# Kernel tuning notes

Measured on AMD Instinct MI355X. Metric: run time of the kernel, lower is better.

The kernel has to match this reference:

```python
import jax, jax.numpy as jnp
import numpy as np

NUM_BINS = 8
C_OUT = 64
CA_RED = 8  # channel-attention reduction (CBAM default-style)


def _bn(x, g, b):
    # BatchNorm1d in training mode: batch statistics, eps=1e-3
    mu = x.mean(0)
    var = x.var(0)
    return (x - mu) / jnp.sqrt(var + 1e-3) * g + b


def setup_inputs() -> dict:
    key = jax.random.key(0)
    ks = jax.random.split(key, 20)
    Nv, U = 400000, 200000
    s = 0.05
    inp = {
        'voxel_features': jax.random.normal(ks[0], (Nv, 5), jnp.float32),
        'voxel_features_coords': jax.random.randint(ks[1], (Nv, 4), 0, NUM_BINS),
        'v_feat_unq_coords': jax.random.randint(ks[2], (U,), 0, 1000000),
        'v_feat_unq_inv': jax.random.randint(ks[3], (Nv,), 0, U),
        'v_feat_unq_cnt': jax.random.randint(ks[4], (U,), 0, 5),
        # up_dimension: Linear(5,32)+ReLU, Linear(32,64)
        'up_w1': jax.random.normal(ks[5], (5, C_OUT // 2), jnp.float32) * s,
        'up_b1': jnp.zeros((C_OUT // 2,), jnp.float32),
        'up_w2': jax.random.normal(ks[6], (C_OUT // 2, C_OUT), jnp.float32) * s,
        'up_b2': jnp.zeros((C_OUT,), jnp.float32),
        # ZBAM (CBAM-1d): channel-attention shared MLP + spatial conv k=7
        'ca_w1': jax.random.normal(ks[7], (C_OUT, C_OUT // CA_RED), jnp.float32) * s,
        'ca_w2': jax.random.normal(ks[8], (C_OUT // CA_RED, C_OUT), jnp.float32) * s,
        'sa_conv': jax.random.normal(ks[9], (1, 2, 7), jnp.float32) * s,  # OIH
        # bin_shuffle: Linear(512,256,no bias)+BN+ReLU, Linear(256,64,no bias)+BN+ReLU
        'bs_w1': jax.random.normal(ks[10], (C_OUT * NUM_BINS, C_OUT * NUM_BINS // 2), jnp.float32) * s,
        'bn1_g': jnp.ones((C_OUT * NUM_BINS // 2,), jnp.float32),
        'bn1_b': jnp.zeros((C_OUT * NUM_BINS // 2,), jnp.float32),
        'bs_w2': jax.random.normal(ks[11], (C_OUT * NUM_BINS // 2, C_OUT), jnp.float32) * s,
        'bn2_g': jnp.ones((C_OUT,), jnp.float32),
        'bn2_b': jnp.zeros((C_OUT,), jnp.float32),
    }
    return inp


def reference(voxel_features, voxel_features_coords, v_feat_unq_coords,
              v_feat_unq_inv, v_feat_unq_cnt,
              up_w1, up_b1, up_w2, up_b2,
              ca_w1, ca_w2, sa_conv,
              bs_w1, bn1_g, bn1_b, bs_w2, bn2_g, bn2_b):
    coords = voxel_features_coords
    U = v_feat_unq_coords.shape[0]
    binz = coords[:, 1]
    # --- binning: scatter voxels into (pillar, z-bin) slots ---
    src = jnp.zeros((U, NUM_BINS, 6), jnp.float32)
    src = src.at[v_feat_unq_inv, binz, 1:].set(voxel_features)
    src = src.at[:, :, 0].set(-1.0)
    src = src.at[v_feat_unq_inv, binz, 0].set(coords[:, 0].astype(jnp.float32))
    # --- occupancy mask + compaction (eager nonzero) ---
    idx = jnp.nonzero(v_feat_unq_cnt >= 2)[0]
    src = src[idx]                      # (N, P=8, 6)
    feat = src[:, :, 1:]                # (N, 8, 5)
    # --- up_dimension MLP ---
    h = jnp.maximum(feat @ up_w1 + up_b1, 0.0) @ up_w2 + up_b2  # (N, 8, 64)
    x = jnp.swapaxes(h, 1, 2)           # (N, C=64, P=8)
    # --- ZBAM: CBAM-style channel + spatial attention over z-bins ---
    def ca_mlp(v):
        return jnp.maximum(v @ ca_w1, 0.0) @ ca_w2
    ca = jax.nn.sigmoid(ca_mlp(x.mean(-1)) + ca_mlp(x.max(-1)))  # (N, C)
    x = x * ca[:, :, None]
    sa_in = jnp.stack([x.mean(1), x.max(1)], axis=1)             # (N, 2, P)
    sa = jax.lax.conv_general_dilated(sa_in, sa_conv, (1,), [(3, 3)],
                                      dimension_numbers=('NCH', 'OIH', 'NCH'))
    x = x * jax.nn.sigmoid(sa)          # (N, C, P)
    # --- bin_shuffle: flatten (C,P) row-major as torch .view does ---
    flat = x.reshape(x.shape[0], C_OUT * NUM_BINS)  # (N, 512)
    y = jnp.maximum(_bn(flat @ bs_w1, bn1_g, bn1_b), 0.0)
    y = jnp.maximum(_bn(y @ bs_w2, bn2_g, bn2_b), 0.0)
    return y
```

## Files before the change

kernel.cpp:

```cpp
#include <hip/hip_runtime.h>
#include <cmath>

typedef __attribute__((ext_vector_type(8))) short short8;
typedef __attribute__((ext_vector_type(4))) float f32x4;

__device__ __forceinline__ ushort f2b(float x) {
    union { float f; unsigned u; } v; v.f = x;
    unsigned r = v.u + 0x7FFFu + ((v.u >> 16) & 1u);
    return (ushort)(r >> 16);
}
__device__ __forceinline__ float b2f(ushort h) {
    union { unsigned u; float f; } v; v.u = ((unsigned)h) << 16; return v.f;
}
__device__ __forceinline__ float sigm(float x) { return 1.0f / (1.0f + __expf(-x)); }

template <int C>
__device__ __forceinline__ float dppf(float x) {
    return __builtin_bit_cast(float,
        __builtin_amdgcn_update_dpp(0, __builtin_bit_cast(int, x), C, 0xf, 0xf, true));
}
__device__ __forceinline__ float rsum16(float v) {
    v += dppf<0x140>(v);
    v += dppf<0x141>(v);
    v += dppf<0x1B>(v);
    v += dppf<0xB1>(v);
    return v;
}
__device__ __forceinline__ float rmax16(float v) {
    v = fmaxf(v, dppf<0x140>(v));
    v = fmaxf(v, dppf<0x141>(v));
    v = fmaxf(v, dppf<0x1B>(v));
    v = fmaxf(v, dppf<0xB1>(v));
    return v;
}
__device__ __forceinline__ float swzf16(float x) {
    return __builtin_bit_cast(float,
        __builtin_amdgcn_ds_swizzle(__builtin_bit_cast(int, x), 0x401F));
}
__device__ __forceinline__ unsigned swzu16(unsigned x) {
    return (unsigned)__builtin_amdgcn_ds_swizzle((int)x, 0x401F);
}

#define GL16(g, s) __builtin_amdgcn_global_load_lds( \
    (const __attribute__((address_space(1))) unsigned int*)(g), \
    (__attribute__((address_space(3))) unsigned int*)(s), 16, 0, 0)

__global__ __launch_bounds__(256) void k_prologue(
    const int* __restrict__ inv, const int* __restrict__ coords, int Nv,
    const int* __restrict__ cnt, int U, int* __restrict__ bc, int nbc,
    const float* __restrict__ w1, const float* __restrict__ w2,
    ushort* __restrict__ w1t, ushort* __restrict__ w2t,
    float* __restrict__ ss, int* __restrict__ winner)
{
    int i = blockIdx.x * 256 + threadIdx.x;
    if (i < Nv) {
        int u = inv[i];
        int b = coords[i * 4 + 1];
        atomicMax(&winner[u * 8 + b], i);
    }
    {
        int s = (i < U && cnt[i] >= 2) ? 1 : 0;
        unsigned long long m = __ballot(s);
        __shared__ int wc[4];
        int lane = threadIdx.x & 63, w = threadIdx.x >> 6;
        if (lane == 0) wc[w] = __popcll(m);
        __syncthreads();
        if (threadIdx.x == 0 && blockIdx.x < nbc)
            bc[blockIdx.x] = wc[0] + wc[1] + wc[2] + wc[3];
    }
    if (i < 512 * 256) {
        int n = i >> 9, k = i & 511;
        w1t[i] = f2b(w1[k * 256 + n]);
    }
    int j = i - 512 * 256;
    if (j >= 0 && j < 256 * 64) {
        int n = j >> 8, k = j & 255;
        w2t[j] = f2b(w2[k * 64 + n]);
    }
    if (i < 640) ss[i] = 0.0f;
}

__global__ __launch_bounds__(256) void k_write_sel(
    const int* __restrict__ cnt, int U,
    const int* __restrict__ bc, int* __restrict__ sel)
{
    int i = blockIdx.x * 256 + threadIdx.x;
    int s = (i < U && cnt[i] >= 2) ? 1 : 0;
    unsigned long long m = __ballot(s);
    __shared__ int wc[4], wsum[4];
    int lane = threadIdx.x & 63, w = threadIdx.x >> 6;
    if (lane == 0) wc[w] = __popcll(m);
    int part = 0;
    for (int b = threadIdx.x; b < blockIdx.x; b += 256) part += bc[b];
    #pragma unroll
    for (int o = 1; o < 64; o <<= 1) part += __shfl_xor(part, o);
    if (lane == 0) wsum[w] = part;
    __syncthreads();
    int off = wsum[0] + wsum[1] + wsum[2] + wsum[3];
    for (int jj = 0; jj < w; jj++) off += wc[jj];
    if (s) sel[off + __popcll(m & ((1ull << lane) - 1ull))] = i;
}

__global__ __launch_bounds__(64) void k_feat4(
    const float* __restrict__ vf, const int* __restrict__ winner,
    const int* __restrict__ sel,
    const float* __restrict__ up_w1, const float* __restrict__ up_b1,
    const float* __restrict__ up_w2, const float* __restrict__ up_b2,
    const float* __restrict__ ca_w1, const float* __restrict__ ca_w2,
    const float* __restrict__ sa_conv,
    ushort* __restrict__ xsg, int M, int Mp, int nw)
{
    __shared__ float sfeat[16 * 12];

    const int l   = threadIdx.x;
    const int lr  = l & 15;
    const int lk8 = (l >> 4) * 8;
    const int qsel = (l >> 4) & 1;
    const int rowh = l >> 5;

    float w1v[5][8], b1v[8];
    #pragma unroll
    for (int p = 0; p < 5; p++)
        #pragma unroll
        for (int kk = 0; kk < 8; kk++) w1v[p][kk] = up_w1[p * 32 + lk8 + kk];
    #pragma unroll
    for (int kk = 0; kk < 8; kk++) b1v[kk] = up_b1[lk8 + kk];

    short8 bv[4];
    #pragma unroll
    for (int j = 0; j < 4; j++)
        #pragma unroll
        for (int kk = 0; kk < 8; kk++)
            bv[j][kk] = (short)f2b(up_w2[(lk8 + kk) * 64 + 16 * j + lr]);

    float b2v[4];
    #pragma unroll
    for (int j = 0; j < 4; j++) b2v[j] = up_b2[16 * j + lr];

    const int jjb = qsel * 4;
    float caw1v[4][4];
    #pragma unroll
    for (int j = 0; j < 4; j++)
        #pragma unroll
        for (int o = 0; o < 4; o++)
            caw1v[j][o] = ca_w1[(16 * j + lr) * 8 + jjb + o];
    float caw2v[4][8];
    #pragma unroll
    for (int j = 0; j < 4; j++)
        #pragma unroll
        for (int jj = 0; jj < 8; jj++)
            caw2v[j][jj] = ca_w2[jj * 64 + 16 * j + lr];
    float sas[14];
    #pragma unroll
    for (int k = 0; k < 14; k++) sas[k] = sa_conv[k];

    auto prefetch = [&](int mb, float4& o4, float& o5) {
        int wv = -1;
        if (l < 16) {
            int mm = mb + (l >> 3);
            if (mm < M) wv = winner[sel[mm] * 8 + (l & 7)];
        }
        int wl = __shfl(wv, lr);
        float4 t4 = make_float4(0.f, 0.f, 0.f, 0.f);
        float t5 = 0.f;
        if (wl >= 0) {
            if (l < 16) {
                const float* p = &vf[(size_t)wl * 5];
                t4.x = p[0]; t4.y = p[1]; t4.z = p[2]; t4.w = p[3];
            } else if (l < 32) {
                t5 = vf[(size_t)wl * 5 + 4];
            }
        }
        o4 = t4; o5 = t5;
    };

    const int step = nw * 2;
    int m2 = blockIdx.x * 2;
    float4 pf; float pf5;
    prefetch(m2, pf, pf5);

    for (; m2 < Mp; m2 += step) {
        if (l < 16) *(float4*)&sfeat[lr * 12] = pf;
        else if (l < 32) sfeat[(l & 15) * 12 + 4] = pf5;
        __syncthreads();
        const float4 ff = *(const float4*)&sfeat[lr * 12];
        const float f4e = sfeat[lr * 12 + 4];
        prefetch(m2 + step, pf, pf5);

        float h[8];
        #pragma unroll
        for (int kk = 0; kk < 8; kk++) {
            float a = b1v[kk];
            a = fmaf(ff.x, w1v[0][kk], a);
            a = fmaf(ff.y, w1v[1][kk], a);
            a = fmaf(ff.z, w1v[2][kk], a);
            a = fmaf(ff.w, w1v[3][kk], a);
            a = fmaf(f4e,  w1v[4][kk], a);
            h[kk] = fmaxf(a, 0.0f);
        }
        short8 af;
        #pragma unroll
        for (int kk = 0; kk < 8; kk++) af[kk] = (short)f2b(h[kk]);

        const f32x4 z = {0.f, 0.f, 0.f, 0.f};
        float x[4][4];
        #pragma unroll
        for (int j = 0; j < 4; j++) {
            f32x4 a = __builtin_amdgcn_mfma_f32_16x16x32_bf16(af, bv[j], z, 0, 0, 0);
            #pragma unroll
            for (int q = 0; q < 4; q++) x[j][q] = a[q] + b2v[j];
        }

        float cm[4], cx[4];
        #pragma unroll
        for (int j = 0; j < 4; j++) {
            float s = (x[j][0] + x[j][1]) + (x[j][2] + x[j][3]);
            float mx = fmaxf(fmaxf(x[j][0], x[j][1]), fmaxf(x[j][2], x[j][3]));
            cm[j] = (s + swzf16(s)) * 0.125f;
            cx[j] = fmaxf(mx, swzf16(mx));
        }
        float pm[4], px[4];
        #pragma unroll
        for (int o = 0; o < 4; o++) {
            float a = 0.f, b = 0.f;
            #pragma unroll
            for (int j = 0; j < 4; j++) {
                a = fmaf(cm[j], caw1v[j][o], a);
                b = fmaf(cx[j], caw1v[j][o], b);
            }
            pm[o] = a; px[o] = b;
        }
        float hso[4], hsx[4];
        #pragma unroll
        for (int o = 0; o < 4; o++) {
            float a = rsum16(pm[o]);
            float b = rsum16(px[o]);
            hso[o] = fmaxf(a, 0.f) + fmaxf(b, 0.f);
        }
        #pragma unroll
        for (int o = 0; o < 4; o++) hsx[o] = swzf16(hso[o]);
        float hs[8];
        #pragma unroll
        for (int jj = 0; jj < 8; jj++)
            hs[jj] = ((jj >> 2) == qsel) ? hso[jj & 3] : hsx[jj & 3];
        #pragma unroll
        for (int j = 0; j < 4; j++) {
            float a = 0.f;
            #pragma unroll
            for (int jj = 0; jj < 8; jj++) a = fmaf(hs[jj], caw2v[j][jj], a);
            float cv = sigm(a);
            x[j][0] *= cv; x[j][1] *= cv; x[j][2] *= cv; x[j][3] *= cv;
        }

        float sq[4], mq[4];
        #pragma unroll
        for (int q = 0; q < 4; q++) {
            float s = (x[0][q] + x[1][q]) + (x[2][q] + x[3][q]);
            float mx = fmaxf(fmaxf(x[0][q], x[1][q]), fmaxf(x[2][q], x[3][q]));
            sq[q] = rsum16(s);
            mq[q] = rmax16(mx);
        }
        float sq2[4], mq2[4];
        #pragma unroll
        for (int q = 0; q < 4; q++) { sq2[q] = swzf16(sq[q]); mq2[q] = swzf16(mq[q]); }
        float am[8], ax[8];
        #pragma unroll
        for (int b = 0; b < 8; b++) {
            int q = b & 3;
            bool own = ((b >> 2) == qsel);
            am[b] = (own ? sq[q] : sq2[q]) * (1.0f / 64.0f);
            ax[b] = own ? mq[q] : mq2[q];
        }
        float sg[8];
        #pragma unroll
        for (int b = 0; b < 8; b++) {
            float a = 0.f;
            #pragma unroll
            for (int k = 0; k < 7; k++) {
                const int p = b + k - 3;
                if (p >= 0 && p < 8) {
                    a = fmaf(am[p], sas[k], a);
                    a = fmaf(ax[p], sas[7 + k], a);
                }
            }
            sg[b] = sigm(a);
        }
        #pragma unroll
        for (int q = 0; q < 4; q++) {
            float g = qsel ? sg[4 + q] : sg[q];
            x[0][q] *= g; x[1][q] *= g; x[2][q] *= g; x[3][q] *= g;
        }

        unsigned u0[4], u1[4];
        #pragma unroll
        for (int j = 0; j < 4; j++) {
            u0[j] = (unsigned)f2b(x[j][0]) | ((unsigned)f2b(x[j][1]) << 16);
            u1[j] = (unsigned)f2b(x[j][2]) | ((unsigned)f2b(x[j][3]) << 16);
        }
        unsigned o0[4], o1[4];
        #pragma unroll
        for (int j = 0; j < 4; j++) { o0[j] = swzu16(u0[j]); o1[j] = swzu16(u1[j]); }
        int mrow = m2 + rowh;
        if (qsel == 0 && mrow < Mp) {
            size_t base = (size_t)mrow * 512;
            if (mrow < M) {
                #pragma unroll
                for (int j = 0; j < 4; j++) {
                    uint4 W = make_uint4(u0[j], u1[j], o0[j], o1[j]);
                    *(uint4*)&xsg[base + (16 * j + lr) * 8] = W;
                }
            } else {
                const uint4 Z = make_uint4(0u, 0u, 0u, 0u);
                #pragma unroll
                for (int j = 0; j < 4; j++)
                    *(uint4*)&xsg[base + (16 * j + lr) * 8] = Z;
            }
        }
        __syncthreads();
    }
}

__global__ __launch_bounds__(256) void k_gemm1(
    const ushort* __restrict__ A, const ushort* __restrict__ B,
    ushort* __restrict__ C, float* __restrict__ ss, int Mp)
{
    __shared__ ushort As[128 * 64];
    __shared__ ushort Bs[128 * 64];
    int t = threadIdx.x;
    int m0 = (blockIdx.x >> 1) * 128;
    int n0 = (blockIdx.x & 1) * 128;
    int l = t & 63, w = t >> 6;
    int wr = w >> 1, wc = w & 1;
    int lr = l & 15, lg = l >> 4, lk = lg * 8;
    f32x4 acc[4][4];
    #pragma unroll
    for (int i = 0; i < 4; i++)
        #pragma unroll
        for (int j = 0; j < 4; j++) acc[i][j] = (f32x4){0.f, 0.f, 0.f, 0.f};

    for (int kt = 0; kt < 512; kt += 64) {
        __syncthreads();
        #pragma unroll
        for (int q = 0; q < 4; q++) {
            int idx = q * 256 + t;
            int row = idx >> 3, kc = (idx & 7) * 8;
            int skc = kc ^ ((row & 7) << 3);
            GL16(&A[(size_t)(m0 + row) * 512 + kt + skc], &As[idx * 8]);
            GL16(&B[(size_t)(n0 + row) * 512 + kt + skc], &Bs[idx * 8]);
        }
        __syncthreads();
        #pragma unroll
        for (int s = 0; s < 2; s++) {
            short8 av[4], bvv[4];
            #pragma unroll
            for (int i = 0; i < 4; i++) {
                int row = wr * 64 + i * 16 + lr;
                av[i] = *(short8*)&As[row * 64 + ((s * 32 + lk) ^ ((row & 7) << 3))];
            }
            #pragma unroll
            for (int j = 0; j < 4; j++) {
                int row = wc * 64 + j * 16 + lr;
                bvv[j] = *(short8*)&Bs[row * 64 + ((s * 32 + lk) ^ ((row & 7) << 3))];
            }
            #pragma unroll
            for (int i = 0; i < 4; i++)
                #pragma unroll
                for (int j = 0; j < 4; j++)
                    acc[i][j] = __builtin_amdgcn_mfma_f32_16x16x32_bf16(av[i], bvv[j], acc[i][j], 0, 0, 0);
        }
    }
    int orow = m0 + wr * 64 + lg * 4;
    int ocol = n0 + wc * 64 + lr;
    float csum[4], csq[4];
    #pragma unroll
    for (int j = 0; j < 4; j++) { csum[j] = 0.f; csq[j] = 0.f; }
    #pragma unroll
    for (int i = 0; i < 4; i++)
        #pragma unroll
        for (int j = 0; j < 4; j++)
            #pragma unroll
            for (int q = 0; q < 4; q++) {
                float v = acc[i][j][q];
                C[(size_t)(orow + i * 16 + q) * 256 + ocol + j * 16] = f2b(v);
                csum[j] += v; csq[j] += v * v;
            }
    #pragma unroll
    for (int j = 0; j < 4; j++) {
        csum[j] += __shfl_xor(csum[j], 16); csum[j] += __shfl_xor(csum[j], 32);
        csq[j]  += __shfl_xor(csq[j], 16);  csq[j]  += __shfl_xor(csq[j], 32);
    }
    if (l < 16) {
        #pragma unroll
        for (int j = 0; j < 4; j++) {
            atomicAdd(&ss[ocol + j * 16], csum[j]);
            atomicAdd(&ss[256 + ocol + j * 16], csq[j]);
        }
    }
}

__global__ __launch_bounds__(256) void k_gemm2(
    const ushort* __restrict__ A, const ushort* __restrict__ B,
    const float* __restrict__ ss, const float* __restrict__ bn1_g,
    const float* __restrict__ bn1_b, float invM,
    float* __restrict__ out, float* __restrict__ ss2, int M)
{
    __shared__ ushort As[128 * 64];
    __shared__ ushort Bs[64 * 64];
    __shared__ float s1[512];
    int t = threadIdx.x;
    {
        float mean = ss[t] * invM;
        float var  = ss[256 + t] * invM - mean * mean;
        float sc   = bn1_g[t] * rsqrtf(var + 0.001f);
        s1[t]       = sc;
        s1[256 + t] = bn1_b[t] - mean * sc;
    }
    int m0 = blockIdx.x * 128;
    int l = t & 63, w = t >> 6;
    int wr = w >> 1, wc = w & 1;
    int lr = l & 15, lg = l >> 4, lk = lg * 8;
    f32x4 acc[4][2];
    #pragma unroll
    for (int i = 0; i < 4; i++)
        #pragma unroll
        for (int j = 0; j < 2; j++) acc[i][j] = (f32x4){0.f, 0.f, 0.f, 0.f};

    for (int kt = 0; kt < 256; kt += 64) {
        __syncthreads();
        #pragma unroll
        for (int q = 0; q < 2; q++) {
            int idx = q * 256 + t;
            int row = idx >> 3, kc = (idx & 7) * 8;
            int skc = kc ^ ((row & 7) << 3);
            GL16(&B[(size_t)row * 256 + kt + skc], &Bs[idx * 8]);
        }
        #pragma unroll
        for (int q = 0; q < 4; q++) {
            int idx = q * 256 + t;
            int row = idx >> 3, kc = (idx & 7) * 8;
            uint4 av = *(const uint4*)&A[(size_t)(m0 + row) * 256 + kt + kc];
            ushort* ap = (ushort*)&av;
            uint4 pk;
            unsigned* pkp = (unsigned*)&pk;
            #pragma unroll
            for (int h = 0; h < 4; h++) {
                int k0 = kt + kc + 2 * h;
                float v0 = fmaxf(fmaf(b2f(ap[2*h]),   s1[k0],   s1[256 + k0]),   0.f);
                float v1 = fmaxf(fmaf(b2f(ap[2*h+1]), s1[k0+1], s1[256 + k0+1]), 0.f);
                pkp[h] = (unsigned)f2b(v0) | ((unsigned)f2b(v1) << 16);
            }
            *(uint4*)&As[row * 64 + (kc ^ ((row & 7) << 3))] = pk;
        }
        __syncthreads();
        #pragma unroll
        for (int s = 0; s < 2; s++) {
            short8 av[4], bvv[2];
            #pragma unroll
            for (int i = 0; i < 4; i++) {
                int row = wr * 64 + i * 16 + lr;
                av[i] = *(short8*)&As[row * 64 + ((s * 32 + lk) ^ ((row & 7) << 3))];
            }
            #pragma unroll
            for (int j = 0; j < 2; j++) {
                int row = wc * 32 + j * 16 + lr;
                bvv[j] = *(short8*)&Bs[row * 64 + ((s * 32 + lk) ^ ((row & 7) << 3))];
            }
            #pragma unroll
            for (int i = 0; i < 4; i++)
                #pragma unroll
                for (int j = 0; j < 2; j++)
                    acc[i][j] = __builtin_amdgcn_mfma_f32_16x16x32_bf16(av[i], bvv[j], acc[i][j], 0, 0, 0);
        }
    }
    int orow = m0 + wr * 64 + lg * 4;
    int ocol = wc * 32 + lr;
    float csum[2], csq[2];
    #pragma unroll
    for (int j = 0; j < 2; j++) { csum[j] = 0.f; csq[j] = 0.f; }
    #pragma unroll
    for (int i = 0; i < 4; i++)
        #pragma unroll
        for (int j = 0; j < 2; j++)
            #pragma unroll
            for (int q = 0; q < 4; q++) {
                int rr = orow + i * 16 + q;
                if (rr < M) {
                    float v = acc[i][j][q];
                    out[(size_t)rr * 64 + ocol + j * 16] = v;
                    csum[j] += v; csq[j] += v * v;
                }
            }
    #pragma unroll
    for (int j = 0; j < 2; j++) {
        csum[j] += __shfl_xor(csum[j], 16); csum[j] += __shfl_xor(csum[j], 32);
        csq[j]  += __shfl_xor(csq[j], 16);  csq[j]  += __shfl_xor(csq[j], 32);
    }
    if (l < 16) {
        #pragma unroll
        for (int j = 0; j < 2; j++) {
            atomicAdd(&ss2[ocol + j * 16], csum[j]);
            atomicAdd(&ss2[64 + ocol + j * 16], csq[j]);
        }
    }
}

__global__ __launch_bounds__(256) void k_bn2_apply4(
    float4* __restrict__ out4, const float* __restrict__ ss2,
    const float* __restrict__ bn2_g, const float* __restrict__ bn2_b,
    float invM, int n4)
{
    __shared__ float s2[128];
    if (threadIdx.x < 64) {
        int c = threadIdx.x;
        float mean = ss2[c] * invM;
        float var  = ss2[64 + c] * invM - mean * mean;
        float sc   = bn2_g[c] * rsqrtf(var + 0.001f);
        s2[c]      = sc;
        s2[64 + c] = bn2_b[c] - mean * sc;
    }
    __syncthreads();
    int i = blockIdx.x * 256 + threadIdx.x;
    if (i < n4) {
        float4 v = out4[i];
        int c0 = (i & 15) * 4;
        v.x = fmaxf(fmaf(v.x, s2[c0 + 0], s2[64 + c0 + 0]), 0.f);
        v.y = fmaxf(fmaf(v.y, s2[c0 + 1], s2[64 + c0 + 1]), 0.f);
        v.z = fmaxf(fmaf(v.z, s2[c0 + 2], s2[64 + c0 + 2]), 0.f);
        v.w = fmaxf(fmaf(v.w, s2[c0 + 3], s2[64 + c0 + 3]), 0.f);
        out4[i] = v;
    }
}

extern "C" void kernel_launch(void* const* d_in, const int* in_sizes, int n_in,
                              void* d_out, int out_size, void* d_ws, size_t ws_size,
                              hipStream_t stream) {
    const float* vf     = (const float*)d_in[0];
    const int*   coords = (const int*)d_in[1];
    const int*   inv    = (const int*)d_in[3];
    const int*   cnt    = (const int*)d_in[4];
    const float* up_w1  = (const float*)d_in[5];
    const float* up_b1  = (const float*)d_in[6];
    const float* up_w2  = (const float*)d_in[7];
    const float* up_b2  = (const float*)d_in[8];
    const float* ca_w1  = (const float*)d_in[9];
    const float* ca_w2  = (const float*)d_in[10];
    const float* sa_conv= (const float*)d_in[11];
    const float* bs_w1  = (const float*)d_in[12];
    const float* bn1_g  = (const float*)d_in[13];
    const float* bn1_b  = (const float*)d_in[14];
    const float* bs_w2  = (const float*)d_in[15];
    const float* bn2_g  = (const float*)d_in[16];
    const float* bn2_b  = (const float*)d_in[17];

    int Nv = in_sizes[3];
    int U  = in_sizes[4];
    int M  = out_size / 64;
    int Mp = (M + 127) & ~127;
    float* out = (float*)d_out;

    char* ws = (char*)d_ws;
    auto alloc = [&](size_t bytes) -> char* {
        char* p = ws;
        ws += (bytes + 255) / 256 * 256;
        return p;
    };
    int nb = (U + 255) / 256;
    int*    winner = (int*)alloc((size_t)U * 8 * 4);
    int*    bc     = (int*)alloc((size_t)nb * 4);
    int*    sel    = (int*)alloc((size_t)M * 4);
    float*  ss     = (float*)alloc(640 * 4);
    ushort* w1t    = (ushort*)alloc((size_t)512 * 256 * 2);
    ushort* w2t    = (ushort*)alloc((size_t)256 * 64 * 2);
    ushort* xsg    = (ushort*)alloc((size_t)Mp * 512 * 2);
    ushort* y1     = (ushort*)alloc((size_t)Mp * 256 * 2);

    hipMemsetAsync(winner, 0xFF, (size_t)U * 8 * 4, stream);

    int npro = (Nv + 255) / 256;
    k_prologue<<<npro, 256, 0, stream>>>(inv, coords, Nv, cnt, U, bc, nb,
                                         bs_w1, bs_w2, w1t, w2t, ss, winner);
    k_write_sel<<<nb, 256, 0, stream>>>(cnt, U, bc, sel);

    int nwf = 8192;
    k_feat4<<<nwf, 64, 0, stream>>>(
        vf, winner, sel, up_w1, up_b1, up_w2, up_b2,
        ca_w1, ca_w2, sa_conv, xsg, M, Mp, nwf);

    k_gemm1<<<(Mp / 128) * 2, 256, 0, stream>>>(xsg, w1t, y1, ss, Mp);

    k_gemm2<<<Mp / 128, 256, 0, stream>>>(y1, w2t, ss, bn1_g, bn1_b,
                                          1.0f / (float)M, out, ss + 512, M);

    int n4 = (M * 64) / 4;
    k_bn2_apply4<<<(n4 + 255) / 256, 256, 0, stream>>>(
        (float4*)out, ss + 512, bn2_g, bn2_b, 1.0f / (float)M, n4);
}
```

Measured before the change: 386.8 us.

## Pack feature waves into 256-thread blocks and widen GEMM1 tile to full N

The feature kernel now runs four independent waves per 256-thread block and passes the prefetched voxel features between lanes with shuffles, so the shared-memory staging and both block barriers per iteration go away. GEMM1 switches from two 128x128 blocks per row tile to one 512-thread block covering all 256 output columns. The A tile is then loaded once per row tile rather than twice. The cost is twice as much LDS for the B tile and larger blocks, which may reduce occupancy.

```diff
diff --git a/kernel.cpp b/kernel.cpp
--- a/kernel.cpp
+++ b/kernel.cpp
@@ -101,22 +101,21 @@
     if (s) sel[off + __popcll(m & ((1ull << lane) - 1ull))] = i;
 }
 
-__global__ __launch_bounds__(64) void k_feat4(
+__global__ __launch_bounds__(256) void k_feat5(
     const float* __restrict__ vf, const int* __restrict__ winner,
     const int* __restrict__ sel,
     const float* __restrict__ up_w1, const float* __restrict__ up_b1,
     const float* __restrict__ up_w2, const float* __restrict__ up_b2,
     const float* __restrict__ ca_w1, const float* __restrict__ ca_w2,
     const float* __restrict__ sa_conv,
-    ushort* __restrict__ xsg, int M, int Mp, int nw)
+    ushort* __restrict__ xsg, int M, int Mp, int nwave)
 {
-    __shared__ float sfeat[16 * 12];
-
-    const int l   = threadIdx.x;
-    const int lr  = l & 15;
-    const int lk8 = (l >> 4) * 8;
+    const int l    = threadIdx.x & 63;
+    const int lr   = l & 15;
+    const int lk8  = (l >> 4) * 8;
     const int qsel = (l >> 4) & 1;
     const int rowh = l >> 5;
+    const int gw   = blockIdx.x * 4 + (threadIdx.x >> 6);
 
     float w1v[5][8], b1v[8];
     #pragma unroll
@@ -174,17 +173,16 @@
         o4 = t4; o5 = t5;
     };
 
-    const int step = nw * 2;
-    int m2 = blockIdx.x * 2;
+    const int step = nwave * 2;
+    int m2 = gw * 2;
     float4 pf; float pf5;
     prefetch(m2, pf, pf5);
 
     for (; m2 < Mp; m2 += step) {
-        if (l < 16) *(float4*)&sfeat[lr * 12] = pf;
-        else if (l < 32) sfeat[(l & 15) * 12 + 4] = pf5;
-        __syncthreads();
-        const float4 ff = *(const float4*)&sfeat[lr * 12];
-        const float f4e = sfeat[lr * 12 + 4];
+        float4 ff;
+        ff.x = __shfl(pf.x, lr); ff.y = __shfl(pf.y, lr);
+        ff.z = __shfl(pf.z, lr); ff.w = __shfl(pf.w, lr);
+        float f4e = __shfl(pf5, 16 + lr);
         prefetch(m2 + step, pf, pf5);
 
         float h[8];
@@ -316,21 +314,19 @@
                     *(uint4*)&xsg[base + (16 * j + lr) * 8] = Z;
             }
         }
-        __syncthreads();
-    }
-}
-
-__global__ __launch_bounds__(256) void k_gemm1(
+    }
+}
+
+__global__ __launch_bounds__(512) void k_gemm1(
     const ushort* __restrict__ A, const ushort* __restrict__ B,
     ushort* __restrict__ C, float* __restrict__ ss, int Mp)
 {
     __shared__ ushort As[128 * 64];
-    __shared__ ushort Bs[128 * 64];
+    __shared__ ushort Bs[256 * 64];
     int t = threadIdx.x;
-    int m0 = (blockIdx.x >> 1) * 128;
-    int n0 = (blockIdx.x & 1) * 128;
+    int m0 = blockIdx.x * 128;
     int l = t & 63, w = t >> 6;
-    int wr = w >> 1, wc = w & 1;
+    int wr = w >> 2, wc = w & 3;
     int lr = l & 15, lg = l >> 4, lk = lg * 8;
     f32x4 acc[4][4];
     #pragma unroll
@@ -341,12 +337,18 @@
     for (int kt = 0; kt < 512; kt += 64) {
         __syncthreads();
         #pragma unroll
-        for (int q = 0; q < 4; q++) {
-            int idx = q * 256 + t;
+        for (int q = 0; q < 2; q++) {
+            int idx = q * 512 + t;
             int row = idx >> 3, kc = (idx & 7) * 8;
             int skc = kc ^ ((row & 7) << 3);
             GL16(&A[(size_t)(m0 + row) * 512 + kt + skc], &As[idx * 8]);
-            GL16(&B[(size_t)(n0 + row) * 512 + kt + skc], &Bs[idx * 8]);
+        }
+        #pragma unroll
+        for (int q = 0; q < 4; q++) {
+            int idx = q * 512 + t;
+            int row = idx >> 3, kc = (idx & 7) * 8;
+            int skc = kc ^ ((row & 7) << 3);
+            GL16(&B[(size_t)row * 512 + kt + skc], &Bs[idx * 8]);
         }
         __syncthreads();
         #pragma unroll
@@ -370,7 +372,7 @@
         }
     }
     int orow = m0 + wr * 64 + lg * 4;
-    int ocol = n0 + wc * 64 + lr;
+    int ocol = wc * 64 + lr;
     float csum[4], csq[4];
     #pragma unroll
     for (int j = 0; j < 4; j++) { csum[j] = 0.f; csq[j] = 0.f; }
@@ -581,12 +583,12 @@
                                          bs_w1, bs_w2, w1t, w2t, ss, winner);
     k_write_sel<<<nb, 256, 0, stream>>>(cnt, U, bc, sel);
 
-    int nwf = 8192;
-    k_feat4<<<nwf, 64, 0, stream>>>(
+    int nblk = 2048;
+    k_feat5<<<nblk, 256, 0, stream>>>(
         vf, winner, sel, up_w1, up_b1, up_w2, up_b2,
-        ca_w1, ca_w2, sa_conv, xsg, M, Mp, nwf);
-
-    k_gemm1<<<(Mp / 128) * 2, 256, 0, stream>>>(xsg, w1t, y1, ss, Mp);
+        ca_w1, ca_w2, sa_conv, xsg, M, Mp, nblk * 4);
+
+    k_gemm1<<<Mp / 128, 512, 0, stream>>>(xsg, w1t, y1, ss, Mp);
 
     k_gemm2<<<Mp / 128, 256, 0, stream>>>(y1, w2t, ss, bn1_g, bn1_b,
                                           1.0f / (float)M, out, ss + 512, M);
```

Measured after the change: 384.5 us. About the same (-0.6%).
